# Optimization experiments

Hardware: AMD Instinct MI355X
Metric: run time of the kernel (lower is better)

## Reference

```python
import jax, jax.numpy as jnp
import numpy as np

B = 128        # graphs per batch
N = 512        # nodes per graph (equal-size graphs -> dense mask all True)
F_IN = 128     # dataset.num_features
HID = 128      # hidden
C3 = 3 * HID   # num_layers * hidden (pool in_channels)
HEADS = 5
NC = 2         # num_classes
KC = NC + 1    # num_clusters2 = num_clusters_per_class*(num_classes+1) = 3
NC1 = NC       # num_clusters1 = num_clusters_per_class*num_classes = 2
OUT = 16       # pool out_channels
EPER = 8192    # edges per graph
TAU = 1.0
L1, L2 = 10.0, 0.01
BN_EPS = 1e-5


def setup_inputs() -> dict:
    key = jax.random.key(0)
    ks = jax.random.split(key, 12)
    Nn = B * N
    E = B * EPER
    x = jax.random.normal(ks[0], (Nn, F_IN), jnp.float32)
    local = jax.random.randint(ks[1], (2, E), 0, N)
    off = (jnp.repeat(jnp.arange(B), EPER) * N)[None, :]
    edge_index = (local + off).astype(jnp.int64)  # global node ids, per-graph blocks
    y = jax.random.randint(ks[2], (B,), 0, NC).astype(jnp.int64)

    def w(k_, shp, fan):
        return (jax.random.normal(k_, shp, jnp.float32) / np.sqrt(fan)).astype(jnp.float32)

    params = dict(
        W1=w(ks[3], (F_IN, HID), F_IN), b1=jnp.zeros((HID,), jnp.float32),
        W2=w(ks[4], (HID, HID), HID), b2=jnp.zeros((HID,), jnp.float32),
        W3=w(ks[5], (HID, HID), HID), b3=jnp.zeros((HID,), jnp.float32),
        bn_gamma=jnp.ones((C3,), jnp.float32), bn_beta=jnp.zeros((C3,), jnp.float32),
        k=w(ks[6], (HEADS, KC, C3), C3),
        lin_pool_W=w(ks[7], (C3, OUT), C3),
        lin1_W=w(ks[8], (NC1 * OUT, HID), NC1 * OUT), lin1_b=jnp.zeros((HID,), jnp.float32),
        lin2_W=w(ks[9], (HID, NC), HID), lin2_b=jnp.zeros((NC,), jnp.float32),
    )
    return dict(x=x, edge_index=edge_index, y=y, **params)


def reference(x, edge_index, y, W1, b1, W2, b2, W3, b3, bn_gamma, bn_beta, k,
              lin_pool_W, lin1_W, lin1_b, lin2_W, lin2_b):
    src, dst = edge_index[0], edge_index[1]
    Nn = x.shape[0]

    # GCNConv (normalize=False): out[dst] += (h @ W)[src] ; + bias
    def gcn(h, W, b):
        m = h @ W
        return jnp.zeros_like(m).at[dst].add(m[src]) + b

    h1 = jax.nn.relu(gcn(x, W1, b1))
    h2 = jax.nn.relu(gcn(h1, W2, b2))
    h3 = jax.nn.relu(gcn(h2, W3, b3))
    X = jnp.concatenate([h1, h2, h3], axis=1)  # [Nn, C3]

    # BatchNorm1d (training-mode batch stats, biased var)
    mu = X.mean(0)
    var = X.var(0)
    Xn = (X - mu) / jnp.sqrt(var + BN_EPS) * bn_gamma + bn_beta

    # --- IMPO pool ---
    H, K, C = k.shape
    k2 = k.reshape(H * K, C)
    # squared euclidean cdist: [H*K, Nn]
    d2 = jnp.maximum((k2 ** 2).sum(-1)[:, None] + (Xn ** 2).sum(-1)[None, :]
                     - 2.0 * (k2 @ Xn.T), 0.0)
    dist = (1.0 + d2 / TAU) ** (-(TAU + 1.0) / 2.0)
    dist = dist.reshape(H, K, B, N).transpose(2, 0, 3, 1)  # [B,H,N,K]
    Sh = dist / dist.sum(-1, keepdims=True)
    S = Sh.sum(1)  # sum over heads -> [B,N,K]; mask is all-True

    # per-graph adjacency aggregation: out[row] += S[col], then degree norm
    Sf = S.reshape(Nn, K)
    Sagg = jnp.zeros_like(Sf).at[src].add(Sf[dst])
    deg = (jnp.zeros((Nn,), Sf.dtype).at[src].add(1.0).at[dst].add(1.0)) / 2.0
    deg = jnp.where(deg == 0, 1.0, deg)
    S_raw = (Sagg / deg[:, None]).reshape(B, N, K)

    # use_gumbel=False path: softmax + hard argmax mask
    g = jax.nn.softmax(S_raw, axis=-1)
    onehot = jax.nn.one_hot(jnp.argmax(g, -1), K, dtype=g.dtype)
    Sfin = g * onehot

    xd = Xn.reshape(B, N, C)
    xp = jnp.einsum('bnk,bnc->bkc', Sfin, xd) @ lin_pool_W  # [B,K,OUT]
    out_x = xp[:, :NC1, :]

    # --- impo_loss ---
    yb = jnp.broadcast_to(y[:, None], (B, N))
    assigned = jnp.argmax(Sfin, -1)
    ac = assigned  # cluster_map is identity for num_clusters_per_class=1
    mr = (ac < NC) & (ac == yb)
    mw = (ac < NC) & (ac != yb)
    sum_loss = Sfin.sum(1)[:, :NC1].sum(1).mean()
    mf = (mr | mw).astype(Sfin.dtype)
    counts = jnp.zeros((NC,), Sfin.dtype).at[yb.reshape(-1)].add(mf.reshape(-1))
    bc = jnp.ones((NC,), Sfin.dtype) + counts
    weight = bc.max() / (bc + 0.001)
    logits = Sfin[..., :KC - 1]  # drop last cluster column
    logp = jax.nn.log_softmax(logits, axis=-1)
    ce = -jnp.take_along_axis(logp, yb[..., None], axis=-1)[..., 0]
    wsamp = weight[yb] * mf
    cel = (wsamp * ce).sum() / jnp.maximum(wsamp.sum(), 1e-12)
    total_loss = L1 * cel + L2 * sum_loss

    # head
    xf = out_x.reshape(B, -1)
    xf = jax.nn.relu(xf @ lin1_W + lin1_b)
    out = jax.nn.log_softmax(xf @ lin2_W + lin2_b, axis=-1)
    return (out, total_loss)
```

## Files before the change

kernel.cpp:

```cpp
#include <hip/hip_runtime.h>
#include <hip/hip_bf16.h>

#define BB 128
#define NV 512
#define NN (BB*NV)
#define EPER_C 8192
#define E_TOT (BB*EPER_C)
#define BN_EPS_F 1e-5f

typedef unsigned int u32;
typedef unsigned short u16;

__device__ __forceinline__ float bfu2f_lo(u32 w) { return __uint_as_float(w << 16); }
__device__ __forceinline__ float bfu2f_hi(u32 w) { return __uint_as_float(w & 0xFFFF0000u); }
__device__ __forceinline__ u16 f2bf(float f) {
    u32 u = __float_as_uint(f);
    u32 r = (u + 0x7FFFu + ((u >> 16) & 1u)) >> 16;
    return (u16)r;
}
__device__ __forceinline__ u32 pack2(float a, float b) {
    return (u32)f2bf(a) | ((u32)f2bf(b) << 16);
}
__device__ __forceinline__ float f16u2f(u16 h) {
    const u32 s = ((u32)h & 0x8000u) << 16;
    const u32 e = (h >> 10) & 0x1Fu;
    const u32 m = h & 0x3FFu;
    if (e == 0u) {
        float v = (float)m * 5.9604644775390625e-8f;
        return s ? -v : v;
    }
    if (e == 31u) return __uint_as_float(s | 0x7F800000u | (m << 13));
    return __uint_as_float(s | ((e + 112u) << 23) | (m << 13));
}
__device__ __forceinline__ void u32tof2(u32 w, u32 cls, float& f0, float& f1) {
    if (cls == 2u) { f0 = f16u2f((u16)(w & 0xFFFFu)); f1 = f16u2f((u16)(w >> 16)); }
    else { f0 = bfu2f_lo(w); f1 = bfu2f_hi(w); }
}
__device__ __forceinline__ float san(float v) {
    if (!(v == v)) return 0.f;
    return fminf(fmaxf(v, -1e30f), 1e30f);
}

__device__ __forceinline__ float2 h_ld2(const u32* H, size_t i2, int hf32) {
    float2 v;
    if (hf32) {
        v = ((const float2*)H)[i2];
    } else {
        const u32 w = H[i2];
        v.x = bfu2f_lo(w);
        v.y = bfu2f_hi(w);
    }
    return v;
}
__device__ __forceinline__ void h_st2(u32* H, size_t i2, float a, float b, int hf32) {
    if (hf32) {
        float2 v;
        v.x = a;
        v.y = b;
        ((float2*)H)[i2] = v;
    } else {
        H[i2] = pack2(a, b);
    }
}
__device__ __forceinline__ float h_ld1(const u32* H, size_t i, int hf32) {
    if (hf32) return ((const float*)H)[i];
    return __uint_as_float(((u32)((const u16*)H)[i]) << 16);
}

__global__ void fill_out_kernel(float* o, float v) {
    int i = blockIdx.x * 256 + threadIdx.x;
    if (i < 257) o[i] = v;
}

__global__ void init_kernel(u32* p, int n) {
    int i = blockIdx.x * 256 + threadIdx.x;
    if (i < n) p[i] = 0u;
}

__global__ void probe_kernel(const u32* g, const u32* e, u32* flags) {
    const int t = threadIdx.x;
    u32 acc = 0u;
    for (int i = t; i < 2048; i += 64) acc |= e[2 * i + 1];
#pragma unroll
    for (int s = 32; s > 0; s >>= 1) acc |= (u32)__shfl_xor((int)acc, s);
    if (t == 0) {
        const u32 w = g[0];
        u32 cls = 0u;
        if (w == 0x3F800000u) cls = 1u;
        else if (w == 0x3C003C00u) cls = 2u;
        flags[9] = cls;
        flags[8] = (acc != 0u) ? 1u : 0u;
    }
}

__device__ __forceinline__ int ld_src(const int* e, int is64, size_t i) {
    return (is64 ? e[2 * i] : e[i]) & (NN - 1);
}
__device__ __forceinline__ int ld_dst(const int* e, int is64, size_t i) {
    return (is64 ? e[2 * ((size_t)E_TOT + i)] : e[(size_t)E_TOT + i]) & (NN - 1);
}
__device__ __forceinline__ int ld_y(const int* y, int is64, int bi) {
    return (is64 ? y[2 * bi] : y[bi]) & 1;
}

#define CVT_TOT 66690
struct CvtPtrs { const void* p[14]; };
__global__ __launch_bounds__(256) void cvt_all_kernel(CvtPtrs ptrs, float* __restrict__ dst,
                                                      const u32* __restrict__ flags) {
    const int i = blockIdx.x * 256 + threadIdx.x;
    if (i >= CVT_TOT) return;
    const int kPof[14] = {0, 16384, 16512, 32896, 33024, 49408, 49536, 49920,
                          50304, 56064, 62208, 66304, 66432, 66688};
    const void* pp = ptrs.p[0];
    int base = 0;
#pragma unroll
    for (int s2 = 1; s2 < 14; ++s2) {
        if (i >= kPof[s2]) { pp = ptrs.p[s2]; base = kPof[s2]; }
    }
    const int off = i - base;
    const u32 cls = flags[9];
    float v;
    if (cls == 1u) v = ((const float*)pp)[off];
    else if (cls == 2u) v = f16u2f(((const u16*)pp)[off]);
    else v = __uint_as_float(((u32)((const u16*)pp)[off]) << 16);
    dst[i] = v;
}

__global__ __launch_bounds__(256) void csr_kernel(const int* __restrict__ eidx,
                                                  const u32* __restrict__ flags,
                                                  u16* __restrict__ sortedD,
                                                  u32* __restrict__ rpD) {
    __shared__ u32 cntD[512];
    __shared__ u32 offD[512];
    __shared__ u32 p[256];
    const int bi = blockIdx.x;
    const int t = threadIdx.x;
    const int is64 = (flags[8] == 0u);
    for (int i = t; i < 512; i += 256) cntD[i] = 0u;
    __syncthreads();
    const size_t eb = (size_t)bi * EPER_C;
    for (int e = t; e < EPER_C; e += 256) {
        const int dl = ld_dst(eidx, is64, eb + e) & 511;
        atomicAdd(&cntD[dl], 1u);
    }
    __syncthreads();
    const u32 a0 = cntD[2 * t], a1 = cntD[2 * t + 1];
    p[t] = a0 + a1;
    __syncthreads();
    for (int d = 1; d < 256; d <<= 1) {
        u32 va = p[t];
        if (t >= d) va += p[t - d];
        __syncthreads();
        p[t] = va;
        __syncthreads();
    }
    {
        const u32 exD = p[t] - (a0 + a1);
        offD[2 * t] = exD;
        offD[2 * t + 1] = exD + a0;
    }
    __syncthreads();
    for (int i = t; i < 512; i += 256) rpD[bi * 513 + i] = offD[i];
    if (t == 0) rpD[bi * 513 + 512] = EPER_C;
    for (int i = t; i < 512; i += 256) cntD[i] = 0u;
    __syncthreads();
    for (int e = t; e < EPER_C; e += 256) {
        const int sl = ld_src(eidx, is64, eb + e) & 511;
        const int dl = ld_dst(eidx, is64, eb + e) & 511;
        const u32 pos = offD[dl] + atomicAdd(&cntD[dl], 1u);
        sortedD[eb + pos] = (u16)sl;
    }
}

__global__ __launch_bounds__(256, 2) void gemm_k(const u32* __restrict__ X2,
                                                 const float* __restrict__ Wc,
                                                 u32* __restrict__ Y2,
                                                 const u32* __restrict__ flags,
                                                 int xmode, int hf32) {
    __shared__ float xsT[2][32][132];
    __shared__ float ws[2][32][128];
    const int n0 = blockIdx.x * 128;
    const int t = threadIdx.x;
    const int tx = t & 15, ty = t >> 4;
    u32 cls;
    if (xmode) cls = flags[9];
    else cls = hf32 ? 1u : 0u;

    float4 px[4];
    uint4 pxu[2];
    float4 pw[4];

#define GLOADX(kc) do { \
    if (cls == 1u) { \
        const float4* Xf4 = (const float4*)X2; \
_Pragma("unroll") \
        for (int i_ = 0; i_ < 4; ++i_) { \
            const int task = t + i_ * 256; \
            const int r_ = task >> 3, q_ = task & 7; \
            px[i_] = Xf4[(size_t)(n0 + r_) * 32 + (kc) * 8 + q_]; \
        } \
    } else { \
        const uint4* Xu4 = (const uint4*)X2; \
_Pragma("unroll") \
        for (int i_ = 0; i_ < 2; ++i_) { \
            const int task = t + i_ * 256; \
            const int r_ = task >> 2, uq_ = task & 3; \
            pxu[i_] = Xu4[(size_t)(n0 + r_) * 16 + (kc) * 4 + uq_]; \
        } \
    } \
} while (0)

#define GLOADW(kc) do { \
    const float4* Wf4 = (const float4*)Wc; \
_Pragma("unroll") \
    for (int i_ = 0; i_ < 4; ++i_) { \
        const int task = t + i_ * 256; \
        const int kr_ = task >> 5, cq_ = task & 31; \
        pw[i_] = Wf4[(size_t)((kc) * 32 + kr_) * 32 + cq_]; \
    } \
} while (0)

#define SWRITE(bi) do { \
    if (cls == 1u) { \
_Pragma("unroll") \
        for (int i_ = 0; i_ < 4; ++i_) { \
            const int task = t + i_ * 256; \
            const int r_ = task >> 3, q_ = task & 7; \
            xsT[bi][4 * q_ + 0][r_] = px[i_].x; \
            xsT[bi][4 * q_ + 1][r_] = px[i_].y; \
            xsT[bi][4 * q_ + 2][r_] = px[i_].z; \
            xsT[bi][4 * q_ + 3][r_] = px[i_].w; \
        } \
    } else { \
_Pragma("unroll") \
        for (int i_ = 0; i_ < 2; ++i_) { \
            const int task = t + i_ * 256; \
            const int r_ = task >> 2, uq_ = task & 3; \
            const u32* wp_ = (const u32*)&pxu[i_]; \
_Pragma("unroll") \
            for (int m_ = 0; m_ < 4; ++m_) { \
                float f0_, f1_; \
                u32tof2(wp_[m_], cls, f0_, f1_); \
                xsT[bi][uq_ * 8 + 2 * m_ + 0][r_] = f0_; \
                xsT[bi][uq_ * 8 + 2 * m_ + 1][r_] = f1_; \
            } \
        } \
    } \
_Pragma("unroll") \
    for (int i_ = 0; i_ < 4; ++i_) { \
        const int task = t + i_ * 256; \
        const int kr_ = task >> 5, cq_ = task & 31; \
        *(float4*)&ws[bi][kr_][4 * cq_] = pw[i_]; \
    } \
} while (0)

    GLOADX(0);
    GLOADW(0);
    SWRITE(0);
    __syncthreads();

    float a[2][4][2][4];
#pragma unroll
    for (int rh = 0; rh < 2; ++rh)
#pragma unroll
        for (int j = 0; j < 4; ++j)
#pragma unroll
            for (int ch = 0; ch < 2; ++ch)
#pragma unroll
                for (int i = 0; i < 4; ++i) a[rh][j][ch][i] = 0.f;

    for (int c = 0; c < 4; ++c) {
        if (c < 3) {
            GLOADX(c + 1);
            GLOADW(c + 1);
        }
        const float (*xb)[132] = xsT[c & 1];
        const float (*wb)[128] = ws[c & 1];
#pragma unroll 8
        for (int k = 0; k < 32; ++k) {
            const float4 xa = *(const float4*)&xb[k][4 * ty];
            const float4 xc = *(const float4*)&xb[k][64 + 4 * ty];
            const float4 wa = *(const float4*)&wb[k][4 * tx];
            const float4 wc = *(const float4*)&wb[k][64 + 4 * tx];
            const float xr0[4] = {xa.x, xa.y, xa.z, xa.w};
            const float xr1[4] = {xc.x, xc.y, xc.z, xc.w};
#pragma unroll
            for (int j = 0; j < 4; ++j) {
                a[0][j][0][0] += xr0[j] * wa.x;
                a[0][j][0][1] += xr0[j] * wa.y;
                a[0][j][0][2] += xr0[j] * wa.z;
                a[0][j][0][3] += xr0[j] * wa.w;
                a[0][j][1][0] += xr0[j] * wc.x;
                a[0][j][1][1] += xr0[j] * wc.y;
                a[0][j][1][2] += xr0[j] * wc.z;
                a[0][j][1][3] += xr0[j] * wc.w;
                a[1][j][0][0] += xr1[j] * wa.x;
                a[1][j][0][1] += xr1[j] * wa.y;
                a[1][j][0][2] += xr1[j] * wa.z;
                a[1][j][0][3] += xr1[j] * wa.w;
                a[1][j][1][0] += xr1[j] * wc.x;
                a[1][j][1][1] += xr1[j] * wc.y;
                a[1][j][1][2] += xr1[j] * wc.z;
                a[1][j][1][3] += xr1[j] * wc.w;
            }
        }
        if (c < 3) {
            SWRITE((c + 1) & 1);
            __syncthreads();
        }
    }
#undef GLOADX
#undef GLOADW
#undef SWRITE

#pragma unroll
    for (int rh = 0; rh < 2; ++rh) {
#pragma unroll
        for (int j = 0; j < 4; ++j) {
            const size_t n = (size_t)n0 + rh * 64 + 4 * ty + j;
#pragma unroll
            for (int ch = 0; ch < 2; ++ch) {
                if (hf32) {
                    float4 o;
                    o.x = a[rh][j][ch][0];
                    o.y = a[rh][j][ch][1];
                    o.z = a[rh][j][ch][2];
                    o.w = a[rh][j][ch][3];
                    ((float4*)Y2)[n * 32 + ch * 16 + tx] = o;
                } else {
                    Y2[n * 64 + ch * 32 + 2 * tx + 0] = pack2(a[rh][j][ch][0], a[rh][j][ch][1]);
                    Y2[n * 64 + ch * 32 + 2 * tx + 1] = pack2(a[rh][j][ch][2], a[rh][j][ch][3]);
                }
            }
        }
    }
}

__global__ __launch_bounds__(1024) void gcn_lds_k(const u16* __restrict__ sortedD,
                                                  const u32* __restrict__ rpD,
                                                  const float* __restrict__ bias,
                                                  u32* __restrict__ M2,
                                                  float* __restrict__ bnacc,
                                                  int col_base, int hf32) {
    __shared__ float Ms[512 * 64];
    __shared__ u32 srt32[EPER_C / 2];
    __shared__ u32 rp[513];
    const int t = threadIdx.x;
    const int bi = blockIdx.x >> 1;
    const int hf = blockIdx.x & 1;
    const size_t rowbase = (size_t)bi * 512;
    const u16* srt = (const u16*)srt32;

    const u32* srcw = (const u32*)(sortedD + (size_t)bi * EPER_C);
    for (int i = t; i < EPER_C / 2; i += 1024) srt32[i] = srcw[i];
    for (int i = t; i < 513; i += 1024) rp[i] = rpD[bi * 513 + i];

    if (hf32) {
        const float4* src4 = (const float4*)M2;
        float4* dst4 = (float4*)Ms;
        for (int idx = t; idx < 512 * 16; idx += 1024) {
            const int r = idx >> 4, q = idx & 15;
            dst4[r * 16 + q] = src4[(rowbase + r) * 32 + hf * 16 + q];
        }
    } else {
        for (int idx = t; idx < 512 * 32; idx += 1024) {
            const int r = idx >> 5, q = idx & 31;
            const u32 w = M2[(rowbase + r) * 64 + hf * 32 + q];
            Ms[r * 64 + 2 * q] = bfu2f_lo(w);
            Ms[r * 64 + 2 * q + 1] = bfu2f_hi(w);
        }
    }
    __syncthreads();

    const int j = t & 15;
    const int g = t >> 4;
    const float4* M4 = (const float4*)Ms;
    const float bx = bias[hf * 64 + j * 4 + 0];
    const float by = bias[hf * 64 + j * 4 + 1];
    const float bz = bias[hf * 64 + j * 4 + 2];
    const float bw = bias[hf * 64 + j * 4 + 3];
    float S0 = 0.f, S1 = 0.f, S2 = 0.f, S3 = 0.f;
    float Q0 = 0.f, Q1 = 0.f, Q2 = 0.f, Q3 = 0.f;

#pragma unroll
    for (int gi = 0; gi < 8; ++gi) {
        const int l = g + gi * 64;
        u32 r1 = rp[l + 1];
        if (r1 > EPER_C) r1 = EPER_C;
        u32 r0 = rp[l];
        if (r0 > r1) r0 = r1;
        float ax = 0.f, ay = 0.f, az = 0.f, aw = 0.f;
        u32 idx = r0;
        for (; idx + 4 <= r1; idx += 4) {
            const int sa = srt[idx];
            const int sb = srt[idx + 1];
            const int sc = srt[idx + 2];
            const int sd = srt[idx + 3];
            const float4 va = M4[sa * 16 + j];
            const float4 vb = M4[sb * 16 + j];
            const float4 vc = M4[sc * 16 + j];
            const float4 vd = M4[sd * 16 + j];
            ax += va.x + vb.x; ay += va.y + vb.y; az += va.z + vb.z; aw += va.w + vb.w;
            ax += vc.x + vd.x; ay += vc.y + vd.y; az += vc.z + vd.z; aw += vc.w + vd.w;
        }
        for (; idx < r1; ++idx) {
            const int sa = srt[idx];
            const float4 va = M4[sa * 16 + j];
            ax += va.x; ay += va.y; az += va.z; aw += va.w;
        }
        float vx = san(ax + bx); vx = vx > 0.f ? vx : 0.f;
        float vy = san(ay + by); vy = vy > 0.f ? vy : 0.f;
        float vz = san(az + bz); vz = vz > 0.f ? vz : 0.f;
        float vw = san(aw + bw); vw = vw > 0.f ? vw : 0.f;
        if (hf32) {
            float4 o; o.x = vx; o.y = vy; o.z = vz; o.w = vw;
            ((float4*)M2)[(rowbase + l) * 32 + hf * 16 + j] = o;
        } else {
            const size_t pr = (rowbase + l) * 64 + hf * 32 + 2 * j;
            M2[pr] = pack2(vx, vy);
            M2[pr + 1] = pack2(vz, vw);
        }
        S0 += vx; S1 += vy; S2 += vz; S3 += vw;
        Q0 += vx * vx; Q1 += vy * vy; Q2 += vz * vz; Q3 += vw * vw;
    }

    S0 += __shfl_xor(S0, 16); Q0 += __shfl_xor(Q0, 16);
    S1 += __shfl_xor(S1, 16); Q1 += __shfl_xor(Q1, 16);
    S2 += __shfl_xor(S2, 16); Q2 += __shfl_xor(Q2, 16);
    S3 += __shfl_xor(S3, 16); Q3 += __shfl_xor(Q3, 16);
    S0 += __shfl_xor(S0, 32); Q0 += __shfl_xor(Q0, 32);
    S1 += __shfl_xor(S1, 32); Q1 += __shfl_xor(Q1, 32);
    S2 += __shfl_xor(S2, 32); Q2 += __shfl_xor(Q2, 32);
    S3 += __shfl_xor(S3, 32); Q3 += __shfl_xor(Q3, 32);

    __syncthreads();
    float* red = (float*)srt32;
    const int lane = t & 63;
    const int wid = t >> 6;
    if (lane < 16) {
        float* rw = &red[(wid * 16 + j) * 8];
        rw[0] = S0; rw[1] = Q0; rw[2] = S1; rw[3] = Q1;
        rw[4] = S2; rw[5] = Q2; rw[6] = S3; rw[7] = Q3;
    }
    __syncthreads();
    if (t < 128) {
        float s = 0.f;
        for (int w = 0; w < 16; ++w) s += red[w * 128 + t];
        const int jj = t >> 3;
        const int cc = (t >> 1) & 3;
        const int st = t & 1;
        atomicAdd(&bnacc[(size_t)(col_base + hf * 64 + jj * 4 + cc) * 2 + st], s);
    }
}

__global__ __launch_bounds__(384) void bn2_kernel(const float* __restrict__ bnacc,
                                                  const float* __restrict__ gamma,
                                                  const float* __restrict__ beta,
                                                  float* __restrict__ scaleA,
                                                  float* __restrict__ shiftA) {
    const int c = threadIdx.x;
    const float s = bnacc[c * 2 + 0];
    const float s2 = bnacc[c * 2 + 1];
    const float inv_n = 1.f / (float)NN;
    const float mu = san(s * inv_n);
    float var = san(s2 * inv_n - mu * mu);
    var = var > 0.f ? var : 0.f;
    const float sc = san(gamma[c] / sqrtf(var + BN_EPS_F));
    scaleA[c] = sc;
    shiftA[c] = san(beta[c] - mu * sc);
}

__global__ __launch_bounds__(256) void dist_kernel(const u32* __restrict__ h1,
                                                   const u32* __restrict__ h2,
                                                   const u32* __restrict__ h3,
                                                   const float* __restrict__ kc,
                                                   const float* __restrict__ scaleA,
                                                   const float* __restrict__ shiftA,
                                                   float4* __restrict__ Sf4, int hf32) {
    __shared__ float k2f[15 * 384];
    __shared__ float scl[384], shf[384];
    __shared__ float ksq[15];
    const int t = threadIdx.x;
    for (int i = t; i < 15 * 384; i += 256) k2f[i] = kc[i];
    for (int i = t; i < 384; i += 256) {
        scl[i] = scaleA[i];
        shf[i] = shiftA[i];
    }
    __syncthreads();
    if (t < 15) {
        float q = 0.f;
        for (int c2 = 0; c2 < 384; ++c2) {
            const float v = k2f[t * 384 + c2];
            q += v * v;
        }
        ksq[t] = q;
    }
    __syncthreads();
    const int n = blockIdx.x * 128 + (t >> 1);
    const int sub = t & 1;
    float acc[15];
#pragma unroll
    for (int j = 0; j < 15; ++j) acc[j] = 0.f;
    float xq = 0.f;
#pragma unroll
    for (int pL = 0; pL < 3; ++pL) {
        const u32* hp = (pL == 0) ? h1 : (pL == 1) ? h2 : h3;
        for (int q8 = sub; q8 < 16; q8 += 2) {
            float xv[8];
            if (hf32) {
                const float4 va = ((const float4*)hp)[(size_t)n * 32 + q8 * 2 + 0];
                const float4 vb = ((const float4*)hp)[(size_t)n * 32 + q8 * 2 + 1];
                xv[0] = va.x; xv[1] = va.y; xv[2] = va.z; xv[3] = va.w;
                xv[4] = vb.x; xv[5] = vb.y; xv[6] = vb.z; xv[7] = vb.w;
            } else {
                const uint4 w = ((const uint4*)hp)[(size_t)n * 16 + q8];
                xv[0] = bfu2f_lo(w.x); xv[1] = bfu2f_hi(w.x);
                xv[2] = bfu2f_lo(w.y); xv[3] = bfu2f_hi(w.y);
                xv[4] = bfu2f_lo(w.z); xv[5] = bfu2f_hi(w.z);
                xv[6] = bfu2f_lo(w.w); xv[7] = bfu2f_hi(w.w);
            }
            const int c = pL * 128 + q8 * 8;
#pragma unroll
            for (int i = 0; i < 8; ++i) {
                const float x = xv[i] * scl[c + i] + shf[c + i];
                xv[i] = x;
                xq += x * x;
            }
#pragma unroll
            for (int j = 0; j < 15; ++j) {
                const float* kr = &k2f[j * 384 + c];
                float a = acc[j];
#pragma unroll
                for (int i = 0; i < 8; ++i) a += xv[i] * kr[i];
                acc[j] = a;
            }
        }
    }
#pragma unroll
    for (int j = 0; j < 15; ++j) acc[j] += __shfl_xor(acc[j], 1);
    xq += __shfl_xor(xq, 1);
    if (sub == 0) {
        float dist[15];
#pragma unroll
        for (int j = 0; j < 15; ++j) {
            float d2 = san(ksq[j] + xq - 2.f * acc[j]);
            d2 = d2 > 0.f ? d2 : 0.f;
            dist[j] = 1.f / (1.f + d2);
        }
        float S0 = 0.f, S1 = 0.f, S2 = 0.f;
#pragma unroll
        for (int h = 0; h < 5; ++h) {
            const float a = dist[h * 3 + 0], b = dist[h * 3 + 1], cd = dist[h * 3 + 2];
            const float inv = 1.f / fmaxf(a + b + cd, 1e-30f);
            S0 += a * inv;
            S1 += b * inv;
            S2 += cd * inv;
        }
        float4 o;
        o.x = san(S0); o.y = san(S1); o.z = san(S2); o.w = 0.f;
        Sf4[n] = o;
    }
}

__global__ __launch_bounds__(256) void sagg_kernel(const int* __restrict__ eidx,
                                                   const u32* __restrict__ flags,
                                                   const float4* __restrict__ Sf4,
                                                   const int* __restrict__ y,
                                                   int* __restrict__ nodeK,
                                                   float* __restrict__ nodeW,
                                                   float* __restrict__ scal) {
    __shared__ float sacc[512 * 3];
    __shared__ unsigned int degc[512];
    __shared__ float rA[256], rB[256];
    const int bi = blockIdx.x;
    const int t = threadIdx.x;
    const int is64 = (flags[8] == 0u);
    for (int i = t; i < 512 * 3; i += 256) sacc[i] = 0.f;
    for (int i = t; i < 512; i += 256) degc[i] = 0u;
    __syncthreads();
    const size_t eb = (size_t)bi * EPER_C;
    for (int e = t; e < EPER_C; e += 256) {
        const int sg = ld_src(eidx, is64, eb + e);
        const int dg = ld_dst(eidx, is64, eb + e);
        const int sl = sg & 511;
        const int dl = dg & 511;
        const float4 sv = Sf4[dg];
        atomicAdd(&sacc[sl * 3 + 0], sv.x);
        atomicAdd(&sacc[sl * 3 + 1], sv.y);
        atomicAdd(&sacc[sl * 3 + 2], sv.z);
        atomicAdd(&degc[sl], 1u);
        atomicAdd(&degc[dl], 1u);
    }
    __syncthreads();
    float mfAcc = 0.f, slAcc = 0.f;
    for (int l = t; l < 512; l += 256) {
        const float cnt = (float)degc[l];
        const float degf = cnt > 0.f ? cnt * 0.5f : 1.f;
        const float inv = 1.f / degf;
        const float r0 = san(sacc[l * 3 + 0] * inv);
        const float r1 = san(sacc[l * 3 + 1] * inv);
        const float r2 = san(sacc[l * 3 + 2] * inv);
        int am = 0;
        float mx = r0;
        if (r1 > mx) { mx = r1; am = 1; }
        if (r2 > mx) { mx = r2; am = 2; }
        const float e0 = expf(r0 - mx), e1 = expf(r1 - mx), e2 = expf(r2 - mx);
        const float g = san(1.f / (e0 + e1 + e2));
        const int n = bi * 512 + l;
        nodeK[n] = am;
        nodeW[n] = g;
        if (am < 2) {
            mfAcc += 1.f;
            slAcc += g;
        }
    }
    rA[t] = mfAcc;
    rB[t] = slAcc;
    __syncthreads();
    for (int sft = 128; sft > 0; sft >>= 1) {
        if (t < sft) {
            rA[t] += rA[t + sft];
            rB[t] += rB[t + sft];
        }
        __syncthreads();
    }
    if (t == 0) {
        atomicAdd(&scal[ld_y(y, is64, bi)], rA[0]);
        atomicAdd(&scal[2], rB[0]);
    }
}

__global__ __launch_bounds__(256) void ce_kernel(const int* __restrict__ nodeK,
                                                 const float* __restrict__ nodeW,
                                                 const u32* __restrict__ flags,
                                                 const int* __restrict__ y,
                                                 float* __restrict__ scal) {
    const int n = blockIdx.x * 256 + threadIdx.x;
    const int bi = n >> 9;
    const int is64 = (flags[8] == 0u);
    const int kn = nodeK[n];
    float wce = 0.f, wsum = 0.f;
    if (kn >= 0 && kn < 2) {
        const float w = nodeW[n];
        const int yb = ld_y(y, is64, bi);
        const float l0 = (kn == 0) ? w : 0.f;
        const float l1 = (kn == 1) ? w : 0.f;
        const float m = fmaxf(l0, l1);
        const float lz = m + logf(expf(l0 - m) + expf(l1 - m));
        const float ce = lz - ((yb == 0) ? l0 : l1);
        const float bc0 = 1.f + scal[0];
        const float bc1 = 1.f + scal[1];
        const float bmax = fmaxf(bc0, bc1);
        const float wt = bmax / (((yb == 0) ? bc0 : bc1) + 0.001f);
        wce = san(wt * ce);
        wsum = san(wt);
    }
    __shared__ float rA[256], rB[256];
    const int t = threadIdx.x;
    rA[t] = wce;
    rB[t] = wsum;
    __syncthreads();
    for (int sft = 128; sft > 0; sft >>= 1) {
        if (t < sft) {
            rA[t] += rA[t + sft];
            rB[t] += rB[t + sft];
        }
        __syncthreads();
    }
    if (t == 0) {
        atomicAdd(&scal[3], rA[0]);
        atomicAdd(&scal[4], rB[0]);
    }
}

__global__ __launch_bounds__(384) void xp_kernel(const u32* __restrict__ h1,
                                                 const u32* __restrict__ h2,
                                                 const u32* __restrict__ h3,
                                                 const float* __restrict__ scaleA,
                                                 const float* __restrict__ shiftA,
                                                 const int* __restrict__ nodeK,
                                                 const float* __restrict__ nodeW,
                                                 float* __restrict__ xp, int hf32) {
    const int bi = blockIdx.x >> 2;
    const int ch = blockIdx.x & 3;
    const int c = threadIdx.x;
    const u32* harr = (c < 128) ? h1 : (c < 256) ? h2 : h3;
    const int cc = c & 127;
    const float sc = scaleA[c], sh = shiftA[c];
    float a0 = 0.f, a1 = 0.f;
    const int nb = bi * 512 + ch * 128;
    for (int l = 0; l < 128; ++l) {
        const int kn = nodeK[nb + l];
        if (kn >= 0 && kn < 2) {
            const float w = nodeW[nb + l];
            const float xv = h_ld1(harr, (size_t)(nb + l) * 128 + cc, hf32) * sc + sh;
            if (kn == 0) a0 += w * xv; else a1 += w * xv;
        }
    }
    atomicAdd(&xp[((size_t)bi * 2 + 0) * 384 + c], san(a0));
    atomicAdd(&xp[((size_t)bi * 2 + 1) * 384 + c], san(a1));
}

__global__ __launch_bounds__(128) void head_kernel(const float* __restrict__ xp,
                                                   const float* __restrict__ lpW,
                                                   const float* __restrict__ l1W,
                                                   const float* __restrict__ l1b,
                                                   const float* __restrict__ l2W,
                                                   const float* __restrict__ l2b,
                                                   float* __restrict__ outp) {
    const int bi = blockIdx.x;
    const int t = threadIdx.x;
    __shared__ float xfl[32];
    __shared__ float hidl[128];
    if (t < 32) {
        const int kk = t >> 4, o = t & 15;
        const float* xr = xp + ((size_t)bi * 2 + kk) * 384;
        float acc = 0.f;
        for (int c2 = 0; c2 < 384; ++c2) acc += xr[c2] * lpW[c2 * 16 + o];
        xfl[t] = san(acc);
    }
    __syncthreads();
    float acc = l1b[t];
    for (int i = 0; i < 32; ++i) acc += xfl[i] * l1W[i * 128 + t];
    hidl[t] = fmaxf(san(acc), 0.f);
    __syncthreads();
    if (t == 0) {
        float L0 = l2b[0], L1v = l2b[1];
        for (int j = 0; j < 128; ++j) {
            const float h = hidl[j];
            L0 += h * l2W[j * 2 + 0];
            L1v += h * l2W[j * 2 + 1];
        }
        L0 = san(L0); L1v = san(L1v);
        const float m = fmaxf(L0, L1v);
        const float ls = m + logf(expf(L0 - m) + expf(L1v - m));
        outp[bi * 2 + 0] = san(L0 - ls);
        outp[bi * 2 + 1] = san(L1v - ls);
    }
}

__global__ void fin_kernel(const float* __restrict__ scal, float* __restrict__ outp) {
    const float cel = san(scal[3] / fmaxf(scal[4], 1e-12f));
    const float total = san(10.f * cel + 0.01f * (scal[2] / (float)BB));
    outp[BB * 2] = total;
}

extern "C" void kernel_launch(void* const* d_in, const int* in_sizes, int n_in,
                              void* d_out, int out_size, void* d_ws, size_t ws_size,
                              hipStream_t stream) {
    (void)in_sizes; (void)n_in; (void)out_size;
    float* outp = (float*)d_out;

    const size_t tailW = (size_t)NN * 4 + (size_t)NN + (size_t)NN + 98304 + 16 + 768 + 768
                       + 66690 + 128 * 513 + (size_t)E_TOT / 2;
    const size_t needF = 3ull * NN * 128ull * 4ull + tailW * 4ull;
    const size_t needB = 3ull * NN * 128ull * 2ull + tailW * 4ull;
    int hf32;
    if (ws_size >= needF) hf32 = 1;
    else if (ws_size >= needB) hf32 = 0;
    else {
        fill_out_kernel<<<2, 256, 0, stream>>>(outp, 2000.f + (float)(ws_size >> 20));
        return;
    }

    const u32* xw = (const u32*)d_in[0];
    const int* eidx = (const int*)d_in[1];
    const int* y = (const int*)d_in[2];

    const size_t esz = hf32 ? 4u : 2u;
    char* base = (char*)d_ws;
    u32* H1 = (u32*)base;
    u32* H2 = (u32*)(base + (size_t)NN * 128 * esz);
    u32* H3 = (u32*)(base + 2 * (size_t)NN * 128 * esz);
    float* fb = (float*)(base + 3 * (size_t)NN * 128 * esz);
    float4* Sf4 = (float4*)fb;
    float* nodeW = fb + (size_t)NN * 4;
    int* nodeK = (int*)(nodeW + NN);
    float* xp = (float*)(nodeK + NN);
    float* scal = xp + 98304;
    u32* flags = (u32*)scal;
    float* bnacc = scal + 16;
    float* scaleA = bnacc + 768;
    float* shiftA = scaleA + 384;
    float* canon = shiftA + 384;
    u32* rpD = (u32*)(canon + 66690);
    u16* sortedD = (u16*)(rpD + 128 * 513);

    init_kernel<<<388, 256, 0, stream>>>((u32*)xp, 98304 + 16 + 768);
    probe_kernel<<<1, 64, 0, stream>>>((const u32*)d_in[9], (const u32*)eidx, flags);
    csr_kernel<<<BB, 256, 0, stream>>>(eidx, flags, sortedD, rpD);

    CvtPtrs cp;
    for (int i = 0; i < 14; ++i) cp.p[i] = d_in[3 + i];
    cvt_all_kernel<<<(CVT_TOT + 255) / 256, 256, 0, stream>>>(cp, canon, flags);

    gemm_k<<<NN / 128, 256, 0, stream>>>(xw, canon + 0, H1, flags, 1, hf32);
    gcn_lds_k<<<BB * 2, 1024, 0, stream>>>(sortedD, rpD, canon + 16384, H1, bnacc, 0, hf32);
    gemm_k<<<NN / 128, 256, 0, stream>>>(H1, canon + 16512, H2, flags, 0, hf32);
    gcn_lds_k<<<BB * 2, 1024, 0, stream>>>(sortedD, rpD, canon + 32896, H2, bnacc, 128, hf32);
    gemm_k<<<NN / 128, 256, 0, stream>>>(H2, canon + 33024, H3, flags, 0, hf32);
    gcn_lds_k<<<BB * 2, 1024, 0, stream>>>(sortedD, rpD, canon + 49408, H3, bnacc, 256, hf32);
    bn2_kernel<<<1, 384, 0, stream>>>(bnacc, canon + 49536, canon + 49920, scaleA, shiftA);
    dist_kernel<<<NN / 128, 256, 0, stream>>>(H1, H2, H3, canon + 50304, scaleA, shiftA,
                                              Sf4, hf32);
    sagg_kernel<<<BB, 256, 0, stream>>>(eidx, flags, Sf4, y, nodeK, nodeW, scal);
    ce_kernel<<<NN / 256, 256, 0, stream>>>(nodeK, nodeW, flags, y, scal);
    xp_kernel<<<BB * 4, 384, 0, stream>>>(H1, H2, H3, scaleA, shiftA, nodeK, nodeW, xp, hf32);
    head_kernel<<<BB, 128, 0, stream>>>(xp, canon + 56064, canon + 62208, canon + 66304,
                                        canon + 66432, canon + 66688, outp);
    fin_kernel<<<1, 1, 0, stream>>>(scal, outp);
}
```

Before: 463.7 us.

## Vectorize xp pooling kernel with shared weights and factored batch-norm affine

Result: faster. 443.6 us (-4.3%).

```diff
diff --git a/kernel.cpp b/kernel.cpp
--- a/kernel.cpp
+++ b/kernel.cpp
@@ -681,24 +681,67 @@
                                                  const int* __restrict__ nodeK,
                                                  const float* __restrict__ nodeW,
                                                  float* __restrict__ xp, int hf32) {
+    __shared__ float w0s[128], w1s[128];
+    __shared__ float red[4][96][8];
     const int bi = blockIdx.x >> 2;
     const int ch = blockIdx.x & 3;
-    const int c = threadIdx.x;
-    const u32* harr = (c < 128) ? h1 : (c < 256) ? h2 : h3;
-    const int cc = c & 127;
-    const float sc = scaleA[c], sh = shiftA[c];
-    float a0 = 0.f, a1 = 0.f;
+    const int t = threadIdx.x;
     const int nb = bi * 512 + ch * 128;
-    for (int l = 0; l < 128; ++l) {
-        const int kn = nodeK[nb + l];
-        if (kn >= 0 && kn < 2) {
-            const float w = nodeW[nb + l];
-            const float xv = h_ld1(harr, (size_t)(nb + l) * 128 + cc, hf32) * sc + sh;
-            if (kn == 0) a0 += w * xv; else a1 += w * xv;
-        }
-    }
-    atomicAdd(&xp[((size_t)bi * 2 + 0) * 384 + c], san(a0));
-    atomicAdd(&xp[((size_t)bi * 2 + 1) * 384 + c], san(a1));
+    for (int i = t; i < 128; i += 384) {
+        const int kn = nodeK[nb + i];
+        const float w = nodeW[nb + i];
+        w0s[i] = (kn == 0) ? w : 0.f;
+        w1s[i] = (kn == 1) ? w : 0.f;
+    }
+    __syncthreads();
+    const int a = t >> 7;
+    const int l128 = t & 127;
+    const int q = l128 & 31;
+    const int ng = l128 >> 5;
+    const u32* hp = (a == 0) ? h1 : (a == 1) ? h2 : h3;
+    float ax = 0.f, ay = 0.f, az = 0.f, aw = 0.f;
+    float bx = 0.f, by = 0.f, bz = 0.f, bw = 0.f;
+    if (hf32) {
+        const float4* h4 = (const float4*)hp;
+#pragma unroll 8
+        for (int l = ng; l < 128; l += 4) {
+            const float4 v = h4[(size_t)(nb + l) * 32 + q];
+            const float w0 = w0s[l], w1 = w1s[l];
+            ax += w0 * v.x; ay += w0 * v.y; az += w0 * v.z; aw += w0 * v.w;
+            bx += w1 * v.x; by += w1 * v.y; bz += w1 * v.z; bw += w1 * v.w;
+        }
+    } else {
+        const uint2* hu = (const uint2*)hp;
+#pragma unroll 8
+        for (int l = ng; l < 128; l += 4) {
+            const uint2 v = hu[(size_t)(nb + l) * 32 + q];
+            const float w0 = w0s[l], w1 = w1s[l];
+            const float x0 = bfu2f_lo(v.x), x1 = bfu2f_hi(v.x);
+            const float x2 = bfu2f_lo(v.y), x3 = bfu2f_hi(v.y);
+            ax += w0 * x0; ay += w0 * x1; az += w0 * x2; aw += w0 * x3;
+            bx += w1 * x0; by += w1 * x1; bz += w1 * x2; bw += w1 * x3;
+        }
+    }
+    {
+        float* rw = red[ng][a * 32 + q];
+        rw[0] = ax; rw[1] = ay; rw[2] = az; rw[3] = aw;
+        rw[4] = bx; rw[5] = by; rw[6] = bz; rw[7] = bw;
+    }
+    __syncthreads();
+    if (ng == 0) {
+        float sw0 = 0.f, sw1 = 0.f;
+        for (int i = 0; i < 128; ++i) { sw0 += w0s[i]; sw1 += w1s[i]; }
+        const int col0 = a * 128 + q * 4;
+        const int cq = a * 32 + q;
+#pragma unroll
+        for (int m = 0; m < 4; ++m) {
+            const float s0 = red[0][cq][m] + red[1][cq][m] + red[2][cq][m] + red[3][cq][m];
+            const float s1 = red[0][cq][4 + m] + red[1][cq][4 + m] + red[2][cq][4 + m] + red[3][cq][4 + m];
+            const float sc = scaleA[col0 + m], sh = shiftA[col0 + m];
+            atomicAdd(&xp[((size_t)bi * 2 + 0) * 384 + col0 + m], san(sc * s0 + sh * sw0));
+            atomicAdd(&xp[((size_t)bi * 2 + 1) * 384 + col0 + m], san(sc * s1 + sh * sw1));
+        }
+    }
 }
 
 __global__ __launch_bounds__(128) void head_kernel(const float* __restrict__ xp,
```
